# Performance work log

Hardware: AMD Instinct MI355X
Metric: run time of the kernel (lower is better)

The kernel has to match this reference:

```python
import jax, jax.numpy as jnp
import numpy as np

N, E, L, HID, HEADS, G = 50000, 800000, 2, 128, 8, 256
DK = HID // HEADS

def _ln(x, g, b, eps=1e-5):
    m = jnp.mean(x, axis=-1, keepdims=True)
    v = jnp.mean((x - m) ** 2, axis=-1, keepdims=True)
    return (x - m) * jax.lax.rsqrt(v + eps) * g + b

def setup_inputs() -> dict:
    key = jax.random.key(0)
    ks = jax.random.split(key, 24)
    rn = lambda i, s: (0.05 * jax.random.normal(ks[i], s)).astype(jnp.float32)
    return {
        'node_attr': jax.random.randint(ks[0], (N, 4), 0, 64, dtype=jnp.int32),
        'batch_idx': jnp.sort(jax.random.randint(ks[1], (N,), 0, G, dtype=jnp.int32)),
        'edge_index': jax.random.randint(ks[2], (2, E), 0, N, dtype=jnp.int32),
        'strat_dist': jax.random.randint(ks[3], (E,), 0, 32, dtype=jnp.int32),
        'strat_path': jax.random.randint(ks[4], (E,), 0, 16, dtype=jnp.int32),
        'atom_emb': rn(5, (4, 64, HID)),
        'dist_emb': rn(6, (L, 32, HID)),
        'path_emb': rn(7, (L, 16, HID)),
        'Wq': rn(8, (L, HID, HID)), 'bq': rn(9, (L, HID)),
        'Wk': rn(10, (L, HID, HID)), 'bk': rn(11, (L, HID)),
        'Wv': rn(12, (L, HID, HID)), 'bv': rn(13, (L, HID)),
        'Wa': rn(14, (L, HID, HID)), 'ba': rn(15, (L, HID)),
        'ln1_g': jnp.ones((L, HID), jnp.float32), 'ln1_b': jnp.zeros((L, HID), jnp.float32),
        'Wmid': rn(16, (L, HID, 2 * HID)), 'bmid': rn(17, (L, 2 * HID)),
        'Wo': rn(18, (L, 2 * HID, HID)), 'bo': rn(19, (L, HID)),
        'ln2_g': jnp.ones((L, HID), jnp.float32), 'ln2_b': jnp.zeros((L, HID), jnp.float32),
        'W_out': rn(20, (HID, 1)), 'b_out': jnp.zeros((1,), jnp.float32),
    }

def reference(node_attr, batch_idx, edge_index, strat_dist, strat_path,
              atom_emb, dist_emb, path_emb, Wq, bq, Wk, bk, Wv, bv, Wa, ba,
              ln1_g, ln1_b, Wmid, bmid, Wo, bo, ln2_g, ln2_b, W_out, b_out):
    # node encoder: sum of per-feature embeddings (AtomEncoder style)
    x = sum(atom_emb[f][node_attr[:, f]] for f in range(node_attr.shape[1]))  # [N, HID]
    src, tgt = edge_index[0], edge_index[1]  # j (source), i (target)
    inv_sqrt_dk = np.float32(1.0 / np.sqrt(DK))
    for l in range(L):
        # per-edge gather + relational encodings added to the source vector
        s = x[src] + dist_emb[l][strat_dist] + path_emb[l][strat_path]  # [E, HID]
        t = x[tgt]                                                      # [E, HID]
        q = (t @ Wq[l] + bq[l]).reshape(E, HEADS, DK)
        k = (s @ Wk[l] + bk[l]).reshape(E, HEADS, DK)
        v = (s @ Wv[l] + bv[l]).reshape(E, HEADS, DK)
        scores = jnp.sum(q * k, axis=-1) * inv_sqrt_dk  # [E, HEADS]
        # segment softmax keyed on target node id
        smax = jax.ops.segment_max(scores, tgt, num_segments=N)
        ex = jnp.exp(scores - smax[tgt])
        den = jax.ops.segment_sum(ex, tgt, num_segments=N)
        att = ex / (den[tgt] + 1e-16)                   # [E, HEADS]
        msg = (v * att[:, :, None]).reshape(E, HID)
        aggr = jax.ops.segment_sum(msg, tgt, num_segments=N)  # scatter-add
        # update: attn FFN + residual + LayerNorms (dropout is identity in eval)
        h = _ln(jax.nn.gelu(aggr, approximate=False) @ Wa[l] + ba[l] + x, ln1_g[l], ln1_b[l])
        h2 = jax.nn.gelu(h @ Wmid[l] + bmid[l], approximate=False) @ Wo[l] + bo[l]
        x = _ln(h2 + h, ln2_g[l], ln2_b[l])
    # global mean pool per graph, then readout
    cnt = jax.ops.segment_sum(jnp.ones((N,), x.dtype), batch_idx, num_segments=G)
    pooled = jax.ops.segment_sum(x, batch_idx, num_segments=G) / jnp.maximum(cnt, 1.0)[:, None]
    return pooled @ W_out + b_out
```

## Files before the change

### kernel.cpp

```cpp
#include <hip/hip_runtime.h>
#include <hip/hip_bf16.h>
#include <math.h>
#include <stdint.h>

#define N_NODES 50000
#define N_EDGES 800000
#define HID 128
#define NGRAPH 256
#define NLAYER 2
#define CAP 64

#define SCATH 782
#define EHALF 400000

#define CPAD 5

#define ENC_B 3125
#define TKV_B (ENC_B + 1024)
#define RPK_B (TKV_B + 128)
#define PREP_B (RPK_B + 4)

typedef __bf16 bf16x8 __attribute__((ext_vector_type(8)));
typedef __bf16 bf16x2 __attribute__((ext_vector_type(2)));
typedef float f32x4 __attribute__((ext_vector_type(4)));
typedef float f32x2 __attribute__((ext_vector_type(2)));

__device__ __forceinline__ float gelu_f(float v) {
    return 0.5f * v * (1.0f + erff(v * 0.70710678118654752f));
}

__device__ __forceinline__ f32x2 f8lo(uint32_t d) {
    return __builtin_amdgcn_cvt_pk_f32_fp8((int)d, false);
}
__device__ __forceinline__ f32x2 f8hi(uint32_t d) {
    return __builtin_amdgcn_cvt_pk_f32_fp8((int)d, true);
}
__device__ __forceinline__ uint32_t pk4_fp8(float a, float b, float c, float d) {
    int w = __builtin_amdgcn_cvt_pk_fp8_f32(a, b, 0, false);
    w = __builtin_amdgcn_cvt_pk_fp8_f32(c, d, w, true);
    return (uint32_t)w;
}
__device__ __forceinline__ f32x2 bfpair(uint32_t d) {
    f32x2 r;
    r[0] = __uint_as_float(d << 16);
    r[1] = __uint_as_float(d & 0xffff0000u);
    return r;
}

__device__ __forceinline__ void scatter_block(
    int blk, int ebase, int elim,
    const int* __restrict__ tgt, const int* __restrict__ src,
    const int* __restrict__ sd, const int* __restrict__ sp,
    int* __restrict__ cnt, uint32_t* __restrict__ ei) {
    int tid = threadIdx.x;
    int e0 = ebase + blk * 512 + tid;
    int e1 = e0 + 256;
    bool v0 = e0 < elim;
    bool v1 = e1 < elim;
    int t0 = 0, t1 = 0;
    uint32_t p0 = 0, p1 = 0;
    if (v0) {
        t0 = tgt[e0];
        p0 = (uint32_t)src[e0] | ((uint32_t)((sd[e0] << 4) | sp[e0]) << 16);
    }
    if (v1) {
        t1 = tgt[e1];
        p1 = (uint32_t)src[e1] | ((uint32_t)((sd[e1] << 4) | sp[e1]) << 16);
    }
    int r0 = CAP, r1 = CAP;
    if (v0) r0 = atomicAdd(&cnt[t0 << CPAD], 1);
    if (v1) r1 = atomicAdd(&cnt[t1 << CPAD], 1);
    if (v0 && r0 < CAP) ei[(t0 << 6) + r0] = p0;
    if (v1 && r1 < CAP) ei[(t1 << 6) + r1] = p1;
}

__global__ __launch_bounds__(256) void prep_kernel(
    const int* __restrict__ attr, const float* __restrict__ aemb,
    __bf16* __restrict__ xb,
    const float* __restrict__ de, const float* __restrict__ pe,
    const float* __restrict__ Wk, const float* __restrict__ Wv,
    __bf16* __restrict__ tkv,
    const float* __restrict__ Wq, const float* __restrict__ Wa,
    const float* __restrict__ Wmid, const float* __restrict__ Wo,
    __bf16* __restrict__ wqkvf, __bf16* __restrict__ waf,
    __bf16* __restrict__ wmidf, __bf16* __restrict__ wof,
    const int* __restrict__ batch, const float* __restrict__ bout,
    const float* __restrict__ bq, const float* __restrict__ bk,
    const float* __restrict__ bv,
    float* __restrict__ invc, float* __restrict__ outp, float* __restrict__ bqkv,
    const int* __restrict__ tgt, const int* __restrict__ src,
    const int* __restrict__ sd, const int* __restrict__ sp,
    int* __restrict__ cnt, uint32_t* __restrict__ ei) {
    __shared__ float sde[128];
    int b = blockIdx.x;
    int tid = threadIdx.x;
    if (b < SCATH) {
        scatter_block(b, 0, EHALF, tgt, src, sd, sp, cnt, ei);
        return;
    }
    b -= SCATH;
    if (b < ENC_B) {
        int gid = b * 256 + tid;
        int n = gid >> 4;
        int c8 = (gid & 15) << 3;
        const int4 a = *(const int4*)(attr + n * 4);
        const float* r0 = aemb + (size_t)(0 * 64 + a.x) * 128 + c8;
        const float* r1 = aemb + (size_t)(1 * 64 + a.y) * 128 + c8;
        const float* r2 = aemb + (size_t)(2 * 64 + a.z) * 128 + c8;
        const float* r3 = aemb + (size_t)(3 * 64 + a.w) * 128 + c8;
        f32x4 v0a = *(const f32x4*)r0, v0b = *(const f32x4*)(r0 + 4);
        f32x4 v1a = *(const f32x4*)r1, v1b = *(const f32x4*)(r1 + 4);
        f32x4 v2a = *(const f32x4*)r2, v2b = *(const f32x4*)(r2 + 4);
        f32x4 v3a = *(const f32x4*)r3, v3b = *(const f32x4*)(r3 + 4);
        bf16x8 o;
#pragma unroll
        for (int j = 0; j < 4; j++) {
            o[j] = (__bf16)(v0a[j] + v1a[j] + v2a[j] + v3a[j]);
            o[4 + j] = (__bf16)(v0b[j] + v1b[j] + v2b[j] + v3b[j]);
        }
        *(bf16x8*)(xb + (size_t)n * 128 + c8) = o;
    } else if (b < TKV_B) {
        int bb = b - ENC_B;
        int l = bb >> 9;
        int md = bb & 511;
        int dd = md >> 4, pp = md & 15;
        int c = tid;
        if (c < 128) sde[c] = de[l * 4096 + dd * 128 + c] + pe[l * 2048 + pp * 128 + c];
        __syncthreads();
        const float* W = (c < 128) ? (Wk + l * 16384) : (Wv + l * 16384);
        int cc = c & 127;
        float acc = 0.f;
#pragma unroll 4
        for (int k = 0; k < 128; k++) acc = fmaf(sde[k], W[k * 128 + cc], acc);
        tkv[(size_t)bb * 256 + c] = (__bf16)acc;
    } else if (b < RPK_B) {
        int u = (b - TKV_B) * 256 + tid;
        int l = u >> 14, r = u & 16383;
        const float* srcp;
        __bf16* dstp;
        int kg, scol, srcCO;
        if (r < 6144) {
            kg = r / 384;
            int uu = r % 384;
            int sec = uu >> 7, cc = uu & 127;
            scol = ((cc & 15) << 3) | (cc >> 4);
            const float* Ws = (sec == 0) ? Wq : (sec == 1) ? Wk : Wv;
            srcp = Ws + l * 16384;
            srcCO = 128;
            dstp = wqkvf + (size_t)l * 49152 + (size_t)r * 8;
        } else if (r < 8192) {
            int rr = r - 6144;
            kg = rr >> 7;
            int cc = rr & 127;
            scol = ((cc & 15) << 3) | (cc >> 4);
            srcp = Wa + l * 16384;
            srcCO = 128;
            dstp = waf + (size_t)l * 16384 + (size_t)rr * 8;
        } else if (r < 12288) {
            int rr = r - 8192;
            kg = rr >> 8;
            int uu = rr & 255;
            int blk = uu >> 7, cc = uu & 127;
            scol = blk * 128 + (((cc & 15) << 3) | (cc >> 4));
            srcp = Wmid + l * 32768;
            srcCO = 256;
            dstp = wmidf + (size_t)l * 32768 + (size_t)rr * 8;
        } else {
            int rr = r - 12288;
            kg = rr >> 7;
            int cc = rr & 127;
            scol = ((cc & 15) << 3) | (cc >> 4);
            srcp = Wo + l * 32768;
            srcCO = 128;
            dstp = wof + (size_t)l * 32768 + (size_t)rr * 8;
        }
        bf16x8 o;
#pragma unroll
        for (int j = 0; j < 8; j++) o[j] = (__bf16)srcp[(kg * 8 + j) * srcCO + scol];
        *(bf16x8*)dstp = o;
    } else {
        int sb = b - RPK_B;
        if (sb == 0) {
            int g = tid;
            int lo = 0, hi = N_NODES;
            while (lo < hi) { int mid = (lo + hi) >> 1; if (batch[mid] < g) lo = mid + 1; else hi = mid; }
            int start = lo;
            lo = start; hi = N_NODES;
            while (lo < hi) { int mid = (lo + hi) >> 1; if (batch[mid] < g + 1) lo = mid + 1; else hi = mid; }
            int c2 = lo - start;
            invc[g] = 1.0f / fmaxf((float)c2, 1.0f);
            outp[g] = bout[0];
        } else {
            int r = (sb - 1) * 256 + tid;
            int l = r / 384, c = r % 384;
            float v = (c < 128) ? bq[l * 128 + c]
                    : (c < 256) ? bk[l * 128 + c - 128]
                                : bv[l * 128 + c - 256];
            bqkv[r] = v;
        }
    }
}

__global__ __launch_bounds__(256) void qkv_gemm(
    const __bf16* __restrict__ A, const __bf16* __restrict__ Wf,
    const float* __restrict__ bias, __bf16* __restrict__ Qb,
    uint8_t* __restrict__ kv8, int M, int scatN,
    const int* __restrict__ tgt, const int* __restrict__ src,
    const int* __restrict__ sd, const int* __restrict__ sp,
    int* __restrict__ cnt, uint32_t* __restrict__ ei) {
    int tid = threadIdx.x;
    if (blockIdx.x < (unsigned)scatN) {
        scatter_block(blockIdx.x, EHALF, N_EDGES, tgt, src, sd, sp, cnt, ei);
        return;
    }
    int bq = blockIdx.x - scatN;
    int sec = bq % 3;
    int rowblk = bq / 3;
    int lane = tid & 63;
    int wv = tid >> 6;
    int row0 = rowblk * 64 + wv * 16;
    int col0 = sec * 128;
    if (row0 >= M) return;
    int quad = lane >> 4, tq = lane & 15;
    f32x4 acc[8] = {};
#pragma unroll
    for (int k0 = 0; k0 < 128; k0 += 32) {
        int rr = row0 + tq;
        if (rr >= M) rr = M - 1;
        bf16x8 af = *(const bf16x8*)(A + (size_t)rr * 128 + k0 + quad * 8);
#pragma unroll
        for (int nt = 0; nt < 8; nt++) {
            bf16x8 bfr = *(const bf16x8*)(Wf + ((size_t)((k0 >> 3) + quad) * 384 + col0 + nt * 16 + tq) * 8);
            acc[nt] = __builtin_amdgcn_mfma_f32_16x16x32_bf16(af, bfr, acc[nt], 0, 0, 0);
        }
    }
    int cb = tq * 8;
    float bia[8];
#pragma unroll
    for (int t = 0; t < 8; t++) bia[t] = bias[col0 + cb + t];
#pragma unroll
    for (int v = 0; v < 4; v++) {
        int rr = row0 + quad * 4 + v;
        if (rr >= M) continue;
        float val[8];
#pragma unroll
        for (int t = 0; t < 8; t++) val[t] = acc[t][v] + bia[t];
        if (sec == 0) {
            bf16x8 ov;
#pragma unroll
            for (int t = 0; t < 8; t++) ov[t] = (__bf16)val[t];
            *(bf16x8*)(Qb + (size_t)rr * 128 + cb) = ov;
        } else {
            uint2 st;
            st.x = pk4_fp8(val[0], val[1], val[2], val[3]);
            st.y = pk4_fp8(val[4], val[5], val[6], val[7]);
            *(uint2*)(kv8 + (size_t)rr * 256 + (sec - 1) * 128 + cb) = st;
        }
    }
}

template <bool POOL>
__global__ __launch_bounds__(256) void ffn_uber(
    const __bf16* __restrict__ A,
    const __bf16* __restrict__ xres,
    const __bf16* __restrict__ Waf, const float* __restrict__ ba,
    const float* __restrict__ l1g, const float* __restrict__ l1b,
    const __bf16* __restrict__ Wmf, const float* __restrict__ bmid,
    const __bf16* __restrict__ Wof, const float* __restrict__ bo,
    const float* __restrict__ l2g, const float* __restrict__ l2b,
    __bf16* __restrict__ outx,
    const int* __restrict__ batch, const float* __restrict__ invc,
    const float* __restrict__ WoutV, float* __restrict__ outp,
    int M) {
    __shared__ __bf16 hld[4][16][136];
    __shared__ __bf16 smid[4][16][264];
    __shared__ float ps[POOL ? NGRAPH : 1];
    int lane = threadIdx.x & 63;
    int wv = threadIdx.x >> 6;
    int row0 = blockIdx.x * 64 + wv * 16;
    bool active = row0 < M;
    if (POOL) {
        ps[threadIdx.x] = 0.f;
        __syncthreads();
    } else if (!active) {
        return;
    }
    int quad = lane >> 4, tq = lane & 15;
    if (active) {
        int cb = tq * 8;
        {
            f32x4 acc[8] = {};
#pragma unroll
            for (int k0 = 0; k0 < 128; k0 += 32) {
                int rr = row0 + tq;
                if (rr >= M) rr = M - 1;
                bf16x8 af = *(const bf16x8*)(A + (size_t)rr * 128 + k0 + quad * 8);
#pragma unroll
                for (int nt = 0; nt < 8; nt++) {
                    bf16x8 bfr = *(const bf16x8*)(Waf + ((size_t)((k0 >> 3) + quad) * 128 + nt * 16 + tq) * 8);
                    acc[nt] = __builtin_amdgcn_mfma_f32_16x16x32_bf16(af, bfr, acc[nt], 0, 0, 0);
                }
            }
            float bia[8], gv[8], bv2[8];
#pragma unroll
            for (int t = 0; t < 8; t++) {
                bia[t] = ba[cb + t];
                gv[t] = l1g[cb + t];
                bv2[t] = l1b[cb + t];
            }
#pragma unroll
            for (int v = 0; v < 4; v++) {
                int rr = row0 + quad * 4 + v;
                int rc = (rr < M) ? rr : M - 1;
                bf16x8 rv = *(const bf16x8*)(xres + (size_t)rc * 128 + cb);
                float val[8];
#pragma unroll
                for (int t = 0; t < 8; t++) val[t] = acc[t][v] + bia[t] + (float)rv[t];
                float s = 0.f, s2 = 0.f;
#pragma unroll
                for (int t = 0; t < 8; t++) { s += val[t]; s2 = fmaf(val[t], val[t], s2); }
#pragma unroll
                for (int o = 1; o < 16; o <<= 1) {
                    s += __shfl_xor(s, o);
                    s2 += __shfl_xor(s2, o);
                }
                float m = s * (1.0f / 128.0f);
                float var = s2 * (1.0f / 128.0f) - m * m;
                float rs = rsqrtf(var + 1e-5f);
                bf16x8 ov;
#pragma unroll
                for (int t = 0; t < 8; t++) ov[t] = (__bf16)((val[t] - m) * rs * gv[t] + bv2[t]);
                *(bf16x8*)(&hld[wv][quad * 4 + v][cb]) = ov;
            }
        }
        asm volatile("" ::: "memory");
#pragma unroll
        for (int cH = 0; cH < 2; ++cH) {
            f32x4 acc[8] = {};
#pragma unroll
            for (int k0 = 0; k0 < 128; k0 += 32) {
                bf16x8 af = *(const bf16x8*)(&hld[wv][tq][k0 + quad * 8]);
#pragma unroll
                for (int nt = 0; nt < 8; nt++) {
                    bf16x8 bfr = *(const bf16x8*)(Wmf + ((size_t)((k0 >> 3) + quad) * 256 + cH * 128 + nt * 16 + tq) * 8);
                    acc[nt] = __builtin_amdgcn_mfma_f32_16x16x32_bf16(af, bfr, acc[nt], 0, 0, 0);
                }
            }
            int cb2 = cH * 128 + cb;
            float bia[8];
#pragma unroll
            for (int t = 0; t < 8; t++) bia[t] = bmid[cb2 + t];
#pragma unroll
            for (int v = 0; v < 4; v++) {
                bf16x8 ov;
#pragma unroll
                for (int t = 0; t < 8; t++) ov[t] = (__bf16)gelu_f(acc[t][v] + bia[t]);
                *(bf16x8*)(&smid[wv][quad * 4 + v][cb2]) = ov;
            }
        }
        asm volatile("" ::: "memory");
        f32x4 acc[8] = {};
#pragma unroll
        for (int k0 = 0; k0 < 256; k0 += 32) {
            bf16x8 af = *(const bf16x8*)(&smid[wv][tq][k0 + quad * 8]);
#pragma unroll
            for (int nt = 0; nt < 8; nt++) {
                bf16x8 bfr = *(const bf16x8*)(Wof + ((size_t)((k0 >> 3) + quad) * 128 + nt * 16 + tq) * 8);
                acc[nt] = __builtin_amdgcn_mfma_f32_16x16x32_bf16(af, bfr, acc[nt], 0, 0, 0);
            }
        }
        float bia[8], gv[8], bv2[8], wo8[8];
#pragma unroll
        for (int t = 0; t < 8; t++) {
            bia[t] = bo[cb + t];
            gv[t] = l2g[cb + t];
            bv2[t] = l2b[cb + t];
        }
        if (POOL) {
#pragma unroll
            for (int t = 0; t < 8; t++) wo8[t] = WoutV[cb + t];
        }
#pragma unroll
        for (int v = 0; v < 4; v++) {
            int rr = row0 + quad * 4 + v;
            bf16x8 rv = *(const bf16x8*)(&hld[wv][quad * 4 + v][cb]);
            float val[8];
#pragma unroll
            for (int t = 0; t < 8; t++) val[t] = acc[t][v] + bia[t] + (float)rv[t];
            float s = 0.f, s2 = 0.f;
#pragma unroll
            for (int t = 0; t < 8; t++) { s += val[t]; s2 = fmaf(val[t], val[t], s2); }
#pragma unroll
            for (int o = 1; o < 16; o <<= 1) {
                s += __shfl_xor(s, o);
                s2 += __shfl_xor(s2, o);
            }
            float m = s * (1.0f / 128.0f);
            float var = s2 * (1.0f / 128.0f) - m * m;
            float rs = rsqrtf(var + 1e-5f);
#pragma unroll
            for (int t = 0; t < 8; t++) val[t] = (val[t] - m) * rs * gv[t] + bv2[t];
            if (rr >= M) continue;
            if (!POOL) {
                bf16x8 ov;
#pragma unroll
                for (int t = 0; t < 8; t++) ov[t] = (__bf16)val[t];
                *(bf16x8*)(outx + (size_t)rr * 128 + cb) = ov;
            } else {
                float dot = 0.f;
#pragma unroll
                for (int t = 0; t < 8; t++) dot = fmaf(val[t], wo8[t], dot);
#pragma unroll
                for (int o = 1; o < 16; o <<= 1) dot += __shfl_xor(dot, o);
                if (tq == 0) {
                    int g = batch[rr];
                    atomicAdd(&ps[g], dot * invc[g]);
                }
            }
        }
    }
    if (POOL) {
        __syncthreads();
        float pv = ps[threadIdx.x];
        if (pv != 0.f) atomicAdd(&outp[threadIdx.x], pv);
    }
}

__global__ __launch_bounds__(256) void attn_kernel(
    const __bf16* __restrict__ Qb, const uint8_t* __restrict__ kv8,
    const __bf16* __restrict__ tkv,
    const int* __restrict__ cnt, const uint32_t* __restrict__ ei,
    __bf16* __restrict__ outb) {
    __shared__ float red[4][1376];
    int wv = threadIdx.x >> 6;
    int i = blockIdx.x * 4 + wv;
    int lane = threadIdx.x & 63;
    int slot = lane >> 3, h = lane & 7;
    int ch0 = h * 16;
    const uint4* qv = (const uint4*)(Qb + (size_t)i * 128 + ch0);
    uint4 qa = qv[0], qb = qv[1];
    uint32_t qd[8] = {qa.x, qa.y, qa.z, qa.w, qb.x, qb.y, qb.z, qb.w};
    f32x2 qp[8];
#pragma unroll
    for (int j = 0; j < 8; j++) qp[j] = bfpair(qd[j]);
    int deg = cnt[i << CPAD];
    if (deg > CAP) deg = CAP;
    int p0 = i << 6;
    int p1 = p0 + deg;
    float l = 0.f;
    f32x2 ap[8] = {};
    int p = p0 + slot;
    uint32_t w1 = 0, w2 = 0;
    if (p < p1) w1 = ei[p];
    if (p + 8 < p1) w2 = ei[p + 8];
    uint4 kw, vw, t0, t1, u0, u1;
    {
        int j = w1 & 0xffff, md = w1 >> 16;
        const uint8_t* kr = kv8 + (size_t)j * 256 + ch0;
        kw = *(const uint4*)kr;
        vw = *(const uint4*)(kr + 128);
        const __bf16* tr = tkv + md * 256 + ch0;
        t0 = *(const uint4*)tr;
        t1 = *(const uint4*)(tr + 8);
        u0 = *(const uint4*)(tr + 128);
        u1 = *(const uint4*)(tr + 136);
    }
    while (p < p1) {
        uint4 kwn, vwn, t0n, t1n, u0n, u1n;
        {
            int j = w2 & 0xffff, md = w2 >> 16;
            const uint8_t* kr = kv8 + (size_t)j * 256 + ch0;
            kwn = *(const uint4*)kr;
            vwn = *(const uint4*)(kr + 128);
            const __bf16* tr = tkv + md * 256 + ch0;
            t0n = *(const uint4*)tr;
            t1n = *(const uint4*)(tr + 8);
            u0n = *(const uint4*)(tr + 128);
            u1n = *(const uint4*)(tr + 136);
        }
        uint32_t w3 = w2;
        if (p + 16 < p1) w3 = ei[p + 16];
        uint32_t kd[4] = {kw.x, kw.y, kw.z, kw.w};
        uint32_t vd[4] = {vw.x, vw.y, vw.z, vw.w};
        uint32_t td[8] = {t0.x, t0.y, t0.z, t0.w, t1.x, t1.y, t1.z, t1.w};
        uint32_t ud[8] = {u0.x, u0.y, u0.z, u0.w, u1.x, u1.y, u1.z, u1.w};
        f32x2 sa = {0.f, 0.f};
#pragma unroll
        for (int j = 0; j < 4; j++) {
            f32x2 klo = f8lo(kd[j]) + bfpair(td[2 * j]);
            f32x2 khi = f8hi(kd[j]) + bfpair(td[2 * j + 1]);
            sa = qp[2 * j] * klo + sa;
            sa = qp[2 * j + 1] * khi + sa;
        }
        float s = sa[0] + sa[1];
        float pe = __expf(s * 0.25f);
        l += pe;
        f32x2 pp = {pe, pe};
#pragma unroll
        for (int j = 0; j < 4; j++) {
            f32x2 vlo = f8lo(vd[j]) + bfpair(ud[2 * j]);
            f32x2 vhi = f8hi(vd[j]) + bfpair(ud[2 * j + 1]);
            ap[2 * j] = pp * vlo + ap[2 * j];
            ap[2 * j + 1] = pp * vhi + ap[2 * j + 1];
        }
        kw = kwn; vw = vwn; t0 = t0n; t1 = t1n; u0 = u0n; u1 = u1n;
        w2 = w3;
        p += 8;
    }
    float* rw = red[wv] + slot * 172 + 20 * h;
#pragma unroll
    for (int j = 0; j < 8; j++) *(f32x2*)(rw + 2 * j) = ap[j];
    red[wv][slot * 172 + 156 + h] = l;
    asm volatile("" ::: "memory");
    int pc = 2 * lane + 4 * (lane >> 3);
    int hh = lane >> 3;
    float s0 = 0.f, s1 = 0.f, ls = 0.f;
#pragma unroll
    for (int s = 0; s < 8; s++) {
        float2 v = *(const float2*)(red[wv] + s * 172 + pc);
        s0 += v.x;
        s1 += v.y;
        ls += red[wv][s * 172 + 156 + hh];
    }
    float inv = 1.0f / (ls + 1e-16f);
    bf16x2 o2;
    o2[0] = (__bf16)gelu_f(s0 * inv);
    o2[1] = (__bf16)gelu_f(s1 * inv);
    *(bf16x2*)(outb + (size_t)i * 128 + 2 * lane) = o2;
}

extern "C" void kernel_launch(void* const* d_in, const int* in_sizes, int n_in,
                              void* d_out, int out_size, void* d_ws, size_t ws_size,
                              hipStream_t stream) {
    const int N = N_NODES, E = N_EDGES;
    const int* node_attr = (const int*)d_in[0];
    const int* batch_idx = (const int*)d_in[1];
    const int* edge_index = (const int*)d_in[2];
    const int* strat_dist = (const int*)d_in[3];
    const int* strat_path = (const int*)d_in[4];
    const float* atom_emb = (const float*)d_in[5];
    const float* dist_emb = (const float*)d_in[6];
    const float* path_emb = (const float*)d_in[7];
    const float* Wq = (const float*)d_in[8];
    const float* bq = (const float*)d_in[9];
    const float* Wk = (const float*)d_in[10];
    const float* bk = (const float*)d_in[11];
    const float* Wv = (const float*)d_in[12];
    const float* bv = (const float*)d_in[13];
    const float* Wa = (const float*)d_in[14];
    const float* ba = (const float*)d_in[15];
    const float* ln1g = (const float*)d_in[16];
    const float* ln1b = (const float*)d_in[17];
    const float* Wmid = (const float*)d_in[18];
    const float* bmid = (const float*)d_in[19];
    const float* Wo = (const float*)d_in[20];
    const float* bo = (const float*)d_in[21];
    const float* ln2g = (const float*)d_in[22];
    const float* ln2b = (const float*)d_in[23];
    const float* Wout = (const float*)d_in[24];
    const float* bout = (const float*)d_in[25];
    float* out = (float*)d_out;

    const int* src = edge_index;
    const int* tgt = edge_index + E;

    size_t NF = (size_t)N * HID;
    float* invc = (float*)d_ws;
    float* bqkv = invc + 256;
    __bf16* xb = (__bf16*)(bqkv + 768);
    __bf16* Qb = xb + NF;
    __bf16* ab = Qb + NF;
    __bf16* tkv = ab + NF;
    __bf16* wqkvf = tkv + 262144;
    __bf16* waf = wqkvf + 98304;
    __bf16* wmidf = waf + 32768;
    __bf16* wof = wmidf + 65536;
    uint8_t* kv8 = (uint8_t*)(wof + 65536);
    uint32_t* ei = (uint32_t*)(kv8 + (size_t)N * 256);
    int* cnt = (int*)(ei + (size_t)N * CAP);

    hipMemsetAsync(cnt, 0, (size_t)N * 32 * sizeof(int), stream);
    prep_kernel<<<SCATH + PREP_B, 256, 0, stream>>>(
        node_attr, atom_emb, xb,
        dist_emb, path_emb, Wk, Wv, tkv,
        Wq, Wa, Wmid, Wo, wqkvf, waf, wmidf, wof,
        batch_idx, bout, bq, bk, bv, invc, out, bqkv,
        tgt, src, strat_dist, strat_path, cnt, ei);

    const int GB = (N + 63) / 64;
    const int AB = (N + 3) / 4;

    for (int l = 0; l < NLAYER; ++l) {
        int scatN = (l == 0) ? SCATH : 0;
        qkv_gemm<<<scatN + 3 * GB, 256, 0, stream>>>(
            xb, wqkvf + l * 49152, bqkv + l * 384, Qb, kv8, N, scatN,
            tgt, src, strat_dist, strat_path, cnt, ei);

        attn_kernel<<<AB, 256, 0, stream>>>(Qb, kv8, tkv + l * 131072, cnt, ei, ab);

        if (l < NLAYER - 1) {
            ffn_uber<false><<<GB, 256, 0, stream>>>(
                ab, xb, waf + l * 16384, ba + l * 128, ln1g + l * 128, ln1b + l * 128,
                wmidf + l * 32768, bmid + l * 256, wof + l * 32768, bo + l * 128,
                ln2g + l * 128, ln2b + l * 128, xb,
                nullptr, nullptr, nullptr, nullptr, N);
        } else {
            ffn_uber<true><<<GB, 256, 0, stream>>>(
                ab, xb, waf + l * 16384, ba + l * 128, ln1g + l * 128, ln1b + l * 128,
                wmidf + l * 32768, bmid + l * 256, wof + l * 32768, bo + l * 128,
                ln2g + l * 128, ln2b + l * 128, nullptr,
                batch_idx, invc, Wout, out, N);
        }
    }
}
```

Baseline: 380.1 us.

## Fuse QKV projection into node encoder and previous layer's FFN epilogue

```diff
diff --git a/kernel.cpp b/kernel.cpp
--- a/kernel.cpp
+++ b/kernel.cpp
@@ -10,15 +10,12 @@
 #define NLAYER 2
 #define CAP 64
 
-#define SCATH 782
-#define EHALF 400000
-
 #define CPAD 5
 
-#define ENC_B 3125
-#define TKV_B (ENC_B + 1024)
-#define RPK_B (TKV_B + 128)
-#define PREP_B (RPK_B + 4)
+#define SC1 1563
+#define ENCQ_B 782
+#define TKV1_B 1024
+#define PREP1_B (SC1 + ENCQ_B + TKV1_B)
 
 typedef __bf16 bf16x8 __attribute__((ext_vector_type(8)));
 typedef __bf16 bf16x2 __attribute__((ext_vector_type(2)));
@@ -74,67 +71,20 @@
     if (v1 && r1 < CAP) ei[(t1 << 6) + r1] = p1;
 }
 
-__global__ __launch_bounds__(256) void prep_kernel(
-    const int* __restrict__ attr, const float* __restrict__ aemb,
-    __bf16* __restrict__ xb,
-    const float* __restrict__ de, const float* __restrict__ pe,
-    const float* __restrict__ Wk, const float* __restrict__ Wv,
-    __bf16* __restrict__ tkv,
+__global__ __launch_bounds__(256) void prep0_kernel(
     const float* __restrict__ Wq, const float* __restrict__ Wa,
     const float* __restrict__ Wmid, const float* __restrict__ Wo,
+    const float* __restrict__ Wk, const float* __restrict__ Wv,
     __bf16* __restrict__ wqkvf, __bf16* __restrict__ waf,
     __bf16* __restrict__ wmidf, __bf16* __restrict__ wof,
     const int* __restrict__ batch, const float* __restrict__ bout,
     const float* __restrict__ bq, const float* __restrict__ bk,
     const float* __restrict__ bv,
-    float* __restrict__ invc, float* __restrict__ outp, float* __restrict__ bqkv,
-    const int* __restrict__ tgt, const int* __restrict__ src,
-    const int* __restrict__ sd, const int* __restrict__ sp,
-    int* __restrict__ cnt, uint32_t* __restrict__ ei) {
-    __shared__ float sde[128];
+    float* __restrict__ invc, float* __restrict__ outp, float* __restrict__ bqkv) {
     int b = blockIdx.x;
     int tid = threadIdx.x;
-    if (b < SCATH) {
-        scatter_block(b, 0, EHALF, tgt, src, sd, sp, cnt, ei);
-        return;
-    }
-    b -= SCATH;
-    if (b < ENC_B) {
-        int gid = b * 256 + tid;
-        int n = gid >> 4;
-        int c8 = (gid & 15) << 3;
-        const int4 a = *(const int4*)(attr + n * 4);
-        const float* r0 = aemb + (size_t)(0 * 64 + a.x) * 128 + c8;
-        const float* r1 = aemb + (size_t)(1 * 64 + a.y) * 128 + c8;
-        const float* r2 = aemb + (size_t)(2 * 64 + a.z) * 128 + c8;
-        const float* r3 = aemb + (size_t)(3 * 64 + a.w) * 128 + c8;
-        f32x4 v0a = *(const f32x4*)r0, v0b = *(const f32x4*)(r0 + 4);
-        f32x4 v1a = *(const f32x4*)r1, v1b = *(const f32x4*)(r1 + 4);
-        f32x4 v2a = *(const f32x4*)r2, v2b = *(const f32x4*)(r2 + 4);
-        f32x4 v3a = *(const f32x4*)r3, v3b = *(const f32x4*)(r3 + 4);
-        bf16x8 o;
-#pragma unroll
-        for (int j = 0; j < 4; j++) {
-            o[j] = (__bf16)(v0a[j] + v1a[j] + v2a[j] + v3a[j]);
-            o[4 + j] = (__bf16)(v0b[j] + v1b[j] + v2b[j] + v3b[j]);
-        }
-        *(bf16x8*)(xb + (size_t)n * 128 + c8) = o;
-    } else if (b < TKV_B) {
-        int bb = b - ENC_B;
-        int l = bb >> 9;
-        int md = bb & 511;
-        int dd = md >> 4, pp = md & 15;
-        int c = tid;
-        if (c < 128) sde[c] = de[l * 4096 + dd * 128 + c] + pe[l * 2048 + pp * 128 + c];
-        __syncthreads();
-        const float* W = (c < 128) ? (Wk + l * 16384) : (Wv + l * 16384);
-        int cc = c & 127;
-        float acc = 0.f;
-#pragma unroll 4
-        for (int k = 0; k < 128; k++) acc = fmaf(sde[k], W[k * 128 + cc], acc);
-        tkv[(size_t)bb * 256 + c] = (__bf16)acc;
-    } else if (b < RPK_B) {
-        int u = (b - TKV_B) * 256 + tid;
+    if (b < 128) {
+        int u = b * 256 + tid;
         int l = u >> 14, r = u & 16383;
         const float* srcp;
         __bf16* dstp;
@@ -179,7 +129,7 @@
         for (int j = 0; j < 8; j++) o[j] = (__bf16)srcp[(kg * 8 + j) * srcCO + scol];
         *(bf16x8*)dstp = o;
     } else {
-        int sb = b - RPK_B;
+        int sb = b - 128;
         if (sb == 0) {
             int g = tid;
             int lo = 0, hi = N_NODES;
@@ -201,65 +151,113 @@
     }
 }
 
-__global__ __launch_bounds__(256) void qkv_gemm(
-    const __bf16* __restrict__ A, const __bf16* __restrict__ Wf,
-    const float* __restrict__ bias, __bf16* __restrict__ Qb,
-    uint8_t* __restrict__ kv8, int M, int scatN,
+__global__ __launch_bounds__(256) void prep1_kernel(
+    const int* __restrict__ attr, const float* __restrict__ aemb,
+    __bf16* __restrict__ xb,
+    const float* __restrict__ de, const float* __restrict__ pe,
+    const float* __restrict__ Wk, const float* __restrict__ Wv,
+    __bf16* __restrict__ tkv,
+    const __bf16* __restrict__ wqkvf, const float* __restrict__ bqkv,
+    __bf16* __restrict__ Qb, uint8_t* __restrict__ kv8,
     const int* __restrict__ tgt, const int* __restrict__ src,
     const int* __restrict__ sd, const int* __restrict__ sp,
     int* __restrict__ cnt, uint32_t* __restrict__ ei) {
+    __shared__ __bf16 xt[64][136];
+    __shared__ float sde[128];
+    int b = blockIdx.x;
     int tid = threadIdx.x;
-    if (blockIdx.x < (unsigned)scatN) {
-        scatter_block(blockIdx.x, EHALF, N_EDGES, tgt, src, sd, sp, cnt, ei);
+    if (b < SC1) {
+        scatter_block(b, 0, N_EDGES, tgt, src, sd, sp, cnt, ei);
         return;
     }
-    int bq = blockIdx.x - scatN;
-    int sec = bq % 3;
-    int rowblk = bq / 3;
-    int lane = tid & 63;
-    int wv = tid >> 6;
-    int row0 = rowblk * 64 + wv * 16;
-    int col0 = sec * 128;
-    if (row0 >= M) return;
-    int quad = lane >> 4, tq = lane & 15;
-    f32x4 acc[8] = {};
-#pragma unroll
-    for (int k0 = 0; k0 < 128; k0 += 32) {
-        int rr = row0 + tq;
-        if (rr >= M) rr = M - 1;
-        bf16x8 af = *(const bf16x8*)(A + (size_t)rr * 128 + k0 + quad * 8);
-#pragma unroll
-        for (int nt = 0; nt < 8; nt++) {
-            bf16x8 bfr = *(const bf16x8*)(Wf + ((size_t)((k0 >> 3) + quad) * 384 + col0 + nt * 16 + tq) * 8);
-            acc[nt] = __builtin_amdgcn_mfma_f32_16x16x32_bf16(af, bfr, acc[nt], 0, 0, 0);
-        }
-    }
-    int cb = tq * 8;
-    float bia[8];
-#pragma unroll
-    for (int t = 0; t < 8; t++) bia[t] = bias[col0 + cb + t];
-#pragma unroll
-    for (int v = 0; v < 4; v++) {
-        int rr = row0 + quad * 4 + v;
-        if (rr >= M) continue;
-        float val[8];
-#pragma unroll
-        for (int t = 0; t < 8; t++) val[t] = acc[t][v] + bia[t];
-        if (sec == 0) {
-            bf16x8 ov;
-#pragma unroll
-            for (int t = 0; t < 8; t++) ov[t] = (__bf16)val[t];
-            *(bf16x8*)(Qb + (size_t)rr * 128 + cb) = ov;
-        } else {
-            uint2 st;
-            st.x = pk4_fp8(val[0], val[1], val[2], val[3]);
-            st.y = pk4_fp8(val[4], val[5], val[6], val[7]);
-            *(uint2*)(kv8 + (size_t)rr * 256 + (sec - 1) * 128 + cb) = st;
-        }
-    }
-}
-
-template <bool POOL>
+    b -= SC1;
+    if (b < ENCQ_B) {
+        int n0 = b * 64;
+#pragma unroll
+        for (int it = 0; it < 4; ++it) {
+            int task = it * 256 + tid;
+            int nl = task >> 4;
+            int c8 = (task & 15) << 3;
+            int n = n0 + nl;
+            int nc = (n < N_NODES) ? n : N_NODES - 1;
+            const int4 a = *(const int4*)(attr + (size_t)nc * 4);
+            const float* r0 = aemb + (size_t)a.x * 128 + c8;
+            const float* r1 = aemb + (size_t)(64 + a.y) * 128 + c8;
+            const float* r2 = aemb + (size_t)(128 + a.z) * 128 + c8;
+            const float* r3 = aemb + (size_t)(192 + a.w) * 128 + c8;
+            f32x4 v0a = *(const f32x4*)r0, v0b = *(const f32x4*)(r0 + 4);
+            f32x4 v1a = *(const f32x4*)r1, v1b = *(const f32x4*)(r1 + 4);
+            f32x4 v2a = *(const f32x4*)r2, v2b = *(const f32x4*)(r2 + 4);
+            f32x4 v3a = *(const f32x4*)r3, v3b = *(const f32x4*)(r3 + 4);
+            bf16x8 o;
+#pragma unroll
+            for (int j = 0; j < 4; j++) {
+                o[j] = (__bf16)(v0a[j] + v1a[j] + v2a[j] + v3a[j]);
+                o[4 + j] = (__bf16)(v0b[j] + v1b[j] + v2b[j] + v3b[j]);
+            }
+            *(bf16x8*)(&xt[nl][c8]) = o;
+            if (n < N_NODES) *(bf16x8*)(xb + (size_t)n * 128 + c8) = o;
+        }
+        __syncthreads();
+        int lane = tid & 63;
+        int wv = tid >> 6;
+        int quad = lane >> 4, tq = lane & 15;
+        int row0 = n0 + wv * 16;
+        int cb = tq * 8;
+#pragma unroll
+        for (int sec = 0; sec < 3; ++sec) {
+            int col0 = sec * 128;
+            f32x4 acc[8] = {};
+#pragma unroll
+            for (int k0 = 0; k0 < 128; k0 += 32) {
+                bf16x8 af = *(const bf16x8*)(&xt[wv * 16 + tq][k0 + quad * 8]);
+#pragma unroll
+                for (int nt = 0; nt < 8; nt++) {
+                    bf16x8 bfr = *(const bf16x8*)(wqkvf + ((size_t)((k0 >> 3) + quad) * 384 + col0 + nt * 16 + tq) * 8);
+                    acc[nt] = __builtin_amdgcn_mfma_f32_16x16x32_bf16(af, bfr, acc[nt], 0, 0, 0);
+                }
+            }
+            float bia[8];
+#pragma unroll
+            for (int t = 0; t < 8; t++) bia[t] = bqkv[col0 + cb + t];
+#pragma unroll
+            for (int v = 0; v < 4; v++) {
+                int rr = row0 + quad * 4 + v;
+                if (rr >= N_NODES) continue;
+                float val[8];
+#pragma unroll
+                for (int t = 0; t < 8; t++) val[t] = acc[t][v] + bia[t];
+                if (sec == 0) {
+                    bf16x8 ov;
+#pragma unroll
+                    for (int t = 0; t < 8; t++) ov[t] = (__bf16)val[t];
+                    *(bf16x8*)(Qb + (size_t)rr * 128 + cb) = ov;
+                } else {
+                    uint2 st;
+                    st.x = pk4_fp8(val[0], val[1], val[2], val[3]);
+                    st.y = pk4_fp8(val[4], val[5], val[6], val[7]);
+                    *(uint2*)(kv8 + (size_t)rr * 256 + (sec - 1) * 128 + cb) = st;
+                }
+            }
+        }
+    } else {
+        int bb = b - ENCQ_B;
+        int l = bb >> 9;
+        int md = bb & 511;
+        int dd = md >> 4, pp = md & 15;
+        int c = tid;
+        if (c < 128) sde[c] = de[l * 4096 + dd * 128 + c] + pe[l * 2048 + pp * 128 + c];
+        __syncthreads();
+        const float* W = (c < 128) ? (Wk + l * 16384) : (Wv + l * 16384);
+        int cc = c & 127;
+        float acc = 0.f;
+#pragma unroll 4
+        for (int k = 0; k < 128; k++) acc = fmaf(sde[k], W[k * 128 + cc], acc);
+        tkv[(size_t)bb * 256 + c] = (__bf16)acc;
+    }
+}
+
+template <bool POOL, bool QKV>
 __global__ __launch_bounds__(256) void ffn_uber(
     const __bf16* __restrict__ A,
     const __bf16* __restrict__ xres,
@@ -269,6 +267,8 @@
     const __bf16* __restrict__ Wof, const float* __restrict__ bo,
     const float* __restrict__ l2g, const float* __restrict__ l2b,
     __bf16* __restrict__ outx,
+    const __bf16* __restrict__ Wqf, const float* __restrict__ qbias,
+    __bf16* __restrict__ Qb, uint8_t* __restrict__ kv8,
     const int* __restrict__ batch, const float* __restrict__ invc,
     const float* __restrict__ WoutV, float* __restrict__ outp,
     int M) {
@@ -400,21 +400,62 @@
             float rs = rsqrtf(var + 1e-5f);
 #pragma unroll
             for (int t = 0; t < 8; t++) val[t] = (val[t] - m) * rs * gv[t] + bv2[t];
-            if (rr >= M) continue;
             if (!POOL) {
                 bf16x8 ov;
 #pragma unroll
                 for (int t = 0; t < 8; t++) ov[t] = (__bf16)val[t];
-                *(bf16x8*)(outx + (size_t)rr * 128 + cb) = ov;
+                if (QKV) *(bf16x8*)(&hld[wv][quad * 4 + v][cb]) = ov;
+                if (rr < M) *(bf16x8*)(outx + (size_t)rr * 128 + cb) = ov;
             } else {
-                float dot = 0.f;
-#pragma unroll
-                for (int t = 0; t < 8; t++) dot = fmaf(val[t], wo8[t], dot);
-#pragma unroll
-                for (int o = 1; o < 16; o <<= 1) dot += __shfl_xor(dot, o);
-                if (tq == 0) {
-                    int g = batch[rr];
-                    atomicAdd(&ps[g], dot * invc[g]);
+                if (rr < M) {
+                    float dot = 0.f;
+#pragma unroll
+                    for (int t = 0; t < 8; t++) dot = fmaf(val[t], wo8[t], dot);
+#pragma unroll
+                    for (int o = 1; o < 16; o <<= 1) dot += __shfl_xor(dot, o);
+                    if (tq == 0) {
+                        int g = batch[rr];
+                        atomicAdd(&ps[g], dot * invc[g]);
+                    }
+                }
+            }
+        }
+        if (QKV) {
+            asm volatile("" ::: "memory");
+#pragma unroll
+            for (int sec = 0; sec < 3; ++sec) {
+                int col0 = sec * 128;
+                f32x4 qacc[8] = {};
+#pragma unroll
+                for (int k0 = 0; k0 < 128; k0 += 32) {
+                    bf16x8 af = *(const bf16x8*)(&hld[wv][tq][k0 + quad * 8]);
+#pragma unroll
+                    for (int nt = 0; nt < 8; nt++) {
+                        bf16x8 bfr = *(const bf16x8*)(Wqf + ((size_t)((k0 >> 3) + quad) * 384 + col0 + nt * 16 + tq) * 8);
+                        qacc[nt] = __builtin_amdgcn_mfma_f32_16x16x32_bf16(af, bfr, qacc[nt], 0, 0, 0);
+                    }
+                }
+                float qb8[8];
+#pragma unroll
+                for (int t = 0; t < 8; t++) qb8[t] = qbias[col0 + cb + t];
+#pragma unroll
+                for (int v = 0; v < 4; v++) {
+                    int rr = row0 + quad * 4 + v;
+                    if (rr >= M) continue;
+                    float val[8];
+#pragma unroll
+                    for (int t = 0; t < 8; t++) val[t] = qacc[t][v] + qb8[t];
+                    if (sec == 0) {
+                        bf16x8 ov;
+#pragma unroll
+                        for (int t = 0; t < 8; t++) ov[t] = (__bf16)val[t];
+                        *(bf16x8*)(Qb + (size_t)rr * 128 + cb) = ov;
+                    } else {
+                        uint2 st;
+                        st.x = pk4_fp8(val[0], val[1], val[2], val[3]);
+                        st.y = pk4_fp8(val[4], val[5], val[6], val[7]);
+                        *(uint2*)(kv8 + (size_t)rr * 256 + (sec - 1) * 128 + cb) = st;
+                    }
                 }
             }
         }
@@ -580,36 +621,29 @@
     int* cnt = (int*)(ei + (size_t)N * CAP);
 
     hipMemsetAsync(cnt, 0, (size_t)N * 32 * sizeof(int), stream);
-    prep_kernel<<<SCATH + PREP_B, 256, 0, stream>>>(
-        node_attr, atom_emb, xb,
-        dist_emb, path_emb, Wk, Wv, tkv,
-        Wq, Wa, Wmid, Wo, wqkvf, waf, wmidf, wof,
-        batch_idx, bout, bq, bk, bv, invc, out, bqkv,
+    prep0_kernel<<<132, 256, 0, stream>>>(
+        Wq, Wa, Wmid, Wo, Wk, Wv, wqkvf, waf, wmidf, wof,
+        batch_idx, bout, bq, bk, bv, invc, out, bqkv);
+    prep1_kernel<<<PREP1_B, 256, 0, stream>>>(
+        node_attr, atom_emb, xb, dist_emb, path_emb, Wk, Wv, tkv,
+        wqkvf, bqkv, Qb, kv8,
         tgt, src, strat_dist, strat_path, cnt, ei);
 
     const int GB = (N + 63) / 64;
     const int AB = (N + 3) / 4;
 
-    for (int l = 0; l < NLAYER; ++l) {
-        int scatN = (l == 0) ? SCATH : 0;
-        qkv_gemm<<<scatN + 3 * GB, 256, 0, stream>>>(
-            xb, wqkvf + l * 49152, bqkv + l * 384, Qb, kv8, N, scatN,
-            tgt, src, strat_dist, strat_path, cnt, ei);
-
-        attn_kernel<<<AB, 256, 0, stream>>>(Qb, kv8, tkv + l * 131072, cnt, ei, ab);
-
-        if (l < NLAYER - 1) {
-            ffn_uber<false><<<GB, 256, 0, stream>>>(
-                ab, xb, waf + l * 16384, ba + l * 128, ln1g + l * 128, ln1b + l * 128,
-                wmidf + l * 32768, bmid + l * 256, wof + l * 32768, bo + l * 128,
-                ln2g + l * 128, ln2b + l * 128, xb,
-                nullptr, nullptr, nullptr, nullptr, N);
-        } else {
-            ffn_uber<true><<<GB, 256, 0, stream>>>(
-                ab, xb, waf + l * 16384, ba + l * 128, ln1g + l * 128, ln1b + l * 128,
-                wmidf + l * 32768, bmid + l * 256, wof + l * 32768, bo + l * 128,
-                ln2g + l * 128, ln2b + l * 128, nullptr,
-                batch_idx, invc, Wout, out, N);
-        }
-    }
-}
+    attn_kernel<<<AB, 256, 0, stream>>>(Qb, kv8, tkv, cnt, ei, ab);
+    ffn_uber<false, true><<<GB, 256, 0, stream>>>(
+        ab, xb, waf, ba, ln1g, ln1b,
+        wmidf, bmid, wof, bo, ln2g, ln2b, xb,
+        wqkvf + 49152, bqkv + 384, Qb, kv8,
+        nullptr, nullptr, nullptr, nullptr, N);
+
+    attn_kernel<<<AB, 256, 0, stream>>>(Qb, kv8, tkv + 131072, cnt, ei, ab);
+    ffn_uber<true, false><<<GB, 256, 0, stream>>>(
+        ab, xb, waf + 16384, ba + 128, ln1g + 128, ln1b + 128,
+        wmidf + 32768, bmid + 256, wof + 32768, bo + 128, ln2g + 128, ln2b + 128,
+        nullptr,
+        nullptr, nullptr, nullptr, nullptr,
+        batch_idx, invc, Wout, out, N);
+}
```

Result: no change. 382.6 us (+0.6%).
